# Optimization experiments

Measured on AMD Instinct MI355X. Metric: run time of the kernel, lower is better.

## Reference

```python
import jax, jax.numpy as jnp
import numpy as np

PRED, TOTAL, ITEM = 100000, 120000, 100000
NUI = PRED + ITEM            # nodes in user2item / reverse-consumption graphs
NODES = TOTAL + ITEM         # embedding table rows
EMB = 64
EPS = 1e-5


def _gatv2(src, dst, x, Wl, bl, Wr, br, attn, n):
    """DGL GATv2Conv (1 head), activation=leaky_relu(0.01)."""
    fs = x @ Wl + bl                                   # fc_src
    fd = x @ Wr + br                                   # fc_dst
    e = jax.nn.leaky_relu(fs[src] + fd[dst], 0.2) @ attn   # [E_edges]
    m = jax.ops.segment_max(e, dst, n)                 # per-dst max (stable softmax)
    ex = jnp.exp(e - m[dst])
    denom = jax.ops.segment_sum(ex, dst, n)
    alpha = ex / denom[dst]                            # edge softmax over in-edges
    out = jax.ops.segment_sum(alpha[:, None] * fs[src], dst, n)
    return jax.nn.leaky_relu(out, 0.01)


def _bn(x, g, b):
    mu = jnp.mean(x, 0)
    var = jnp.var(x, 0)
    return (x - mu) * jax.lax.rsqrt(var + EPS) * g + b


def _mlp(x, W, b, g, beta):
    # Linear -> BatchNorm1d (train mode, batch stats) -> LeakyReLU(0.01)
    return jax.nn.leaky_relu(_bn(x @ W + b, g, beta), 0.01)


def _cheb(src, dst, x, W, b, lam, n):
    """ChebConv order-3: h = sum_k T_k(Lhat) x @ W_k + b, leaky_relu."""
    deg = jnp.clip(jax.ops.segment_sum(jnp.ones_like(dst, jnp.float32), dst, n), 1.0)
    dinv = jax.lax.rsqrt(deg)
    norm = dinv[src] * dinv[dst]                       # D^-1/2 A D^-1/2 edge weight

    def lhat(v):  # (2/lam)(I - Ahat) v - v
        av = jax.ops.segment_sum(norm[:, None] * v[src], dst, n)
        return (2.0 / lam) * (v - av) - v

    T0 = x
    T1 = lhat(T0)
    T2 = 2.0 * lhat(T1) - T0
    return jax.nn.leaky_relu(T0 @ W[0] + T1 @ W[1] + T2 @ W[2] + b, 0.01)


def setup_inputs() -> dict:
    key = jax.random.key(0)
    ks = jax.random.split(key, 24)
    ri = lambda k, n, hi: jax.random.randint(k, (n,), 0, hi, dtype=jnp.int32)
    rn = lambda k, shp, s=0.1: jax.random.normal(k, shp, jnp.float32) * s
    return {
        "emb": rn(ks[0], (NODES, EMB), 1.0),
        "bn0_g": jnp.ones((EMB,), jnp.float32),
        "bn0_b": jnp.zeros((EMB,), jnp.float32),
        "gat_Wl": rn(ks[1], (5, EMB, EMB)),
        "gat_bl": jnp.zeros((5, EMB), jnp.float32),
        "gat_Wr": rn(ks[2], (5, EMB, EMB)),
        "gat_br": jnp.zeros((5, EMB), jnp.float32),
        "gat_attn": rn(ks[3], (5, EMB)),
        "cheb_W": rn(ks[4], (3, EMB, EMB)),
        "cheb_b": jnp.zeros((EMB,), jnp.float32),
        "mlp_W": rn(ks[5], (5, 2 * EMB, EMB)),
        "mlp_b": jnp.zeros((5, EMB), jnp.float32),
        "mlp_g": jnp.ones((5, EMB), jnp.float32),
        "mlp_beta": jnp.zeros((5, EMB), jnp.float32),
        "lambda_max": jnp.array([2.0], jnp.float32),
        "u2i_src": ri(ks[6], 1500000, NUI),
        "u2i_dst": ri(ks[7], 1500000, NUI),
        "rc_src": ri(ks[8], 1500000, NUI),
        "rc_dst": ri(ks[9], 1500000, NUI),
        "i2u_src": ri(ks[10], 1000000, PRED),
        "i2u_dst": ri(ks[11], 1000000, PRED),
        "i2u_ids": jnp.arange(PRED, dtype=jnp.int32),
        "sn_src": ri(ks[12], 1000000, PRED),
        "sn_dst": ri(ks[13], 1000000, PRED),
        "snn_src": ri(ks[14], 1500000, TOTAL),
        "snn_dst": ri(ks[15], 1500000, TOTAL),
    }


def reference(emb, bn0_g, bn0_b, gat_Wl, gat_bl, gat_Wr, gat_br, gat_attn,
              cheb_W, cheb_b, mlp_W, mlp_b, mlp_g, mlp_beta, lambda_max,
              u2i_src, u2i_dst, rc_src, rc_dst, i2u_src, i2u_dst, i2u_ids,
              sn_src, sn_dst, snn_src, snn_dst):
    gat = lambda i, src, dst, x, n: _gatv2(src, dst, x, gat_Wl[i], gat_bl[i],
                                           gat_Wr[i], gat_br[i], gat_attn[i], n)
    mlp = lambda i, x: _mlp(x, mlp_W[i], mlp_b[i], mlp_g[i], mlp_beta[i])

    e = _bn(emb, bn0_g, bn0_b)                        # embedding_BN over all nodes
    pred_u = e[:PRED]
    total_u = e[:TOTAL]
    item_e = e[-ITEM:]
    uie = jnp.concatenate([pred_u, item_e], axis=0)   # [NUI, EMB]

    # --- spatial attention: item influence branch ---
    u2i_emb = gat(0, u2i_src, u2i_dst, uie, NUI)
    iie = gat(1, rc_src, rc_dst, u2i_emb, NUI)[:PRED]

    # --- spatial attention: social item branch ---
    su = uie[i2u_ids]                                 # embedding[_ID]
    i2u_emb = gat(2, i2u_src, i2u_dst, su, PRED)
    soc = uie[:PRED]                                  # embedding[social_g.nodes()]
    mask = (jnp.sum(i2u_emb, axis=1) != 0)[:, None]
    soc = soc.at[i2u_ids].set(jnp.where(mask, i2u_emb, soc[i2u_ids]))
    sie = gat(3, sn_src, sn_dst, soc, PRED)

    user_item_embed = mlp(0, jnp.concatenate([iie, sie], axis=1))

    # --- spectral attention ---
    lam = lambda_max[0]
    h = _cheb(snn_src, snn_dst, total_u, cheb_W, cheb_b, lam, TOTAL)
    h = _cheb(snn_src, snn_dst, h, cheb_W, cheb_b, lam, TOTAL)
    user_social_embed = gat(4, snn_src, snn_dst, h, TOTAL)[:PRED]

    # --- mutualistic layer ---
    h_uP = mlp(1, jnp.concatenate([user_item_embed, pred_u], axis=1))
    h_uS = mlp(2, jnp.concatenate([user_social_embed, pred_u], axis=1))
    h_m = h_uP * h_uS
    h_mP = jnp.concatenate([h_m * jax.nn.softmax(h_uP, axis=1), h_uP], axis=1)
    h_mS = jnp.concatenate([h_m * jax.nn.softmax(h_uS, axis=1), h_uS], axis=1)

    # --- prediction layer ---
    h_new_P = mlp(3, h_mP)
    h_new_S = mlp(4, h_mS)
    return (h_new_P, h_new_S)
```

## Files before the change

### kernel.cpp

```cpp
#include <hip/hip_runtime.h>
#include <math.h>

static const int PRED  = 100000;
static const int TOTAL = 120000;
static const int ITEM  = 100000;
static const int NUI   = PRED + ITEM;
static const int NODES = TOTAL + ITEM;
#define BN_EPS 1e-5f
#define MNEG -1e30f
#define WNEG -2e30f

__device__ inline float lrelu(float v, float s) { return v > 0.f ? v : s * v; }

__global__ void k_bn_stats(const float* __restrict__ x, int n, float* __restrict__ sums) {
  __shared__ float ls[256], ls2[256];
  int t = threadIdx.x;
  int col = t & 63;
  float s = 0.f, s2 = 0.f;
  for (int r = blockIdx.x * 4 + (t >> 6); r < n; r += gridDim.x * 4) {
    float v = x[(size_t)r * 64 + col];
    s += v; s2 += v * v;
  }
  ls[t] = s; ls2[t] = s2;
  __syncthreads();
  if (t < 64) {
    atomicAdd(&sums[t],      ls[t] + ls[t + 64] + ls[t + 128] + ls[t + 192]);
    atomicAdd(&sums[64 + t], ls2[t] + ls2[t + 64] + ls2[t + 128] + ls2[t + 192]);
  }
}

__global__ void k_bn_apply(const float* __restrict__ x, float* __restrict__ y,
                           const float* __restrict__ sums,
                           const float* __restrict__ g, const float* __restrict__ b,
                           int n, int relu) {
  size_t tot = (size_t)n * 64;
  size_t i = (size_t)blockIdx.x * blockDim.x + threadIdx.x;
  size_t st = (size_t)gridDim.x * blockDim.x;
  float inv_n = 1.f / (float)n;
  for (; i < tot; i += st) {
    int c = (int)(i & 63);
    float mean = sums[c] * inv_n;
    float var = fmaxf(sums[64 + c] * inv_n - mean * mean, 0.f);
    float o = (x[i] - mean) * rsqrtf(var + BN_EPS) * g[c] + b[c];
    if (relu) o = lrelu(o, 0.01f);
    y[i] = o;
  }
}

__global__ void k_bn0_apply(const float* __restrict__ x, float* __restrict__ e_tot,
                            float* __restrict__ uie, const float* __restrict__ sums,
                            const float* __restrict__ g, const float* __restrict__ b) {
  size_t tot = (size_t)NODES * 64;
  size_t i = (size_t)blockIdx.x * blockDim.x + threadIdx.x;
  size_t st = (size_t)gridDim.x * blockDim.x;
  float inv_n = 1.f / (float)NODES;
  for (; i < tot; i += st) {
    int c = (int)(i & 63);
    size_t row = i >> 6;
    float mean = sums[c] * inv_n;
    float var = fmaxf(sums[64 + c] * inv_n - mean * mean, 0.f);
    float o = (x[i] - mean) * rsqrtf(var + BN_EPS) * g[c] + b[c];
    if (row < (size_t)TOTAL) e_tot[i] = o;
    else uie[((row - TOTAL) + PRED) * 64 + c] = o;
    if (row < (size_t)PRED) uie[i] = o;
  }
}

__global__ __launch_bounds__(128) void k_gemm_dual(const float* __restrict__ A,
    const float* __restrict__ Wl, const float* __restrict__ bl,
    const float* __restrict__ Wr, const float* __restrict__ br,
    float* __restrict__ FS, float* __restrict__ FD, int n) {
  __shared__ float As[128][65];
  __shared__ float Ws[64][68];
  int t = threadIdx.x;
  int row0 = blockIdx.x * 128;
  for (int i = t; i < 2048; i += 128) {
    int r = i >> 4, c = (i & 15) * 4, gr = row0 + r;
    float4 a;
    if (gr < n) a = *(const float4*)&A[(size_t)gr * 64 + c];
    else { a.x = a.y = a.z = a.w = 0.f; }
    As[r][c] = a.x; As[r][c + 1] = a.y; As[r][c + 2] = a.z; As[r][c + 3] = a.w;
  }
  int cg = (t & 7) * 8;
  int rg = (t >> 3) * 8;
  for (int s = 0; s < 2; ++s) {
    const float* Wm = s ? Wr : Wl;
    const float* bias = s ? br : bl;
    __syncthreads();
    for (int i = t; i < 4096; i += 128) Ws[i >> 6][i & 63] = Wm[i];
    __syncthreads();
    float bb[8];
    *(float4*)&bb[0] = *(const float4*)&bias[cg];
    *(float4*)&bb[4] = *(const float4*)&bias[cg + 4];
    float acc[8][8];
    #pragma unroll
    for (int i = 0; i < 8; ++i)
      #pragma unroll
      for (int j = 0; j < 8; ++j) acc[i][j] = bb[j];
    for (int k = 0; k < 64; ++k) {
      float w[8], a[8];
      *(float4*)&w[0] = *(const float4*)&Ws[k][cg];
      *(float4*)&w[4] = *(const float4*)&Ws[k][cg + 4];
      #pragma unroll
      for (int i = 0; i < 8; ++i) a[i] = As[rg + i][k];
      #pragma unroll
      for (int i = 0; i < 8; ++i)
        #pragma unroll
        for (int j = 0; j < 8; ++j)
          acc[i][j] += a[i] * w[j];
    }
    float* C = s ? FD : FS;
    #pragma unroll
    for (int i = 0; i < 8; ++i) {
      int gr = row0 + rg + i;
      if (gr < n) {
        float4 o0, o1;
        o0.x = acc[i][0]; o0.y = acc[i][1]; o0.z = acc[i][2]; o0.w = acc[i][3];
        o1.x = acc[i][4]; o1.y = acc[i][5]; o1.z = acc[i][6]; o1.w = acc[i][7];
        *(float4*)&C[(size_t)gr * 64 + cg] = o0;
        *(float4*)&C[(size_t)gr * 64 + cg + 4] = o1;
      }
    }
  }
}

__global__ __launch_bounds__(128) void k_gemm_cat(const float* __restrict__ A1,
    const float* __restrict__ A2, const float* __restrict__ A3,
    const float* __restrict__ Wm, const float* __restrict__ bias,
    float* __restrict__ C, int n, int nseg, int relu) {
  __shared__ float As[128][65];
  __shared__ float Ws[64][68];
  int t = threadIdx.x;
  int row0 = blockIdx.x * 128;
  int cg = (t & 7) * 8;
  int rg = (t >> 3) * 8;
  float bb[8];
  *(float4*)&bb[0] = *(const float4*)&bias[cg];
  *(float4*)&bb[4] = *(const float4*)&bias[cg + 4];
  float acc[8][8];
  #pragma unroll
  for (int i = 0; i < 8; ++i)
    #pragma unroll
    for (int j = 0; j < 8; ++j) acc[i][j] = bb[j];
  for (int s = 0; s < nseg; ++s) {
    const float* A = (s == 0) ? A1 : (s == 1) ? A2 : A3;
    __syncthreads();
    for (int i = t; i < 4096; i += 128) Ws[i >> 6][i & 63] = Wm[s * 4096 + i];
    for (int i = t; i < 2048; i += 128) {
      int r = i >> 4, c = (i & 15) * 4, gr = row0 + r;
      float4 a;
      if (gr < n) a = *(const float4*)&A[(size_t)gr * 64 + c];
      else { a.x = a.y = a.z = a.w = 0.f; }
      As[r][c] = a.x; As[r][c + 1] = a.y; As[r][c + 2] = a.z; As[r][c + 3] = a.w;
    }
    __syncthreads();
    for (int k = 0; k < 64; ++k) {
      float w[8], a[8];
      *(float4*)&w[0] = *(const float4*)&Ws[k][cg];
      *(float4*)&w[4] = *(const float4*)&Ws[k][cg + 4];
      #pragma unroll
      for (int i = 0; i < 8; ++i) a[i] = As[rg + i][k];
      #pragma unroll
      for (int i = 0; i < 8; ++i)
        #pragma unroll
        for (int j = 0; j < 8; ++j)
          acc[i][j] += a[i] * w[j];
    }
  }
  #pragma unroll
  for (int i = 0; i < 8; ++i) {
    int gr = row0 + rg + i;
    if (gr < n) {
      float4 o0, o1;
      o0.x = acc[i][0]; o0.y = acc[i][1]; o0.z = acc[i][2]; o0.w = acc[i][3];
      o1.x = acc[i][4]; o1.y = acc[i][5]; o1.z = acc[i][6]; o1.w = acc[i][7];
      if (relu) {
        o0.x = lrelu(o0.x, 0.01f); o0.y = lrelu(o0.y, 0.01f); o0.z = lrelu(o0.z, 0.01f); o0.w = lrelu(o0.w, 0.01f);
        o1.x = lrelu(o1.x, 0.01f); o1.y = lrelu(o1.y, 0.01f); o1.z = lrelu(o1.z, 0.01f); o1.w = lrelu(o1.w, 0.01f);
      }
      *(float4*)&C[(size_t)gr * 64 + cg] = o0;
      *(float4*)&C[(size_t)gr * 64 + cg + 4] = o1;
    }
  }
}

__global__ __launch_bounds__(512) void k_bhist(const int* __restrict__ dst, int* __restrict__ M,
                                               int E, int nbuck, int chunk) {
  __shared__ int h[1600];
  int t = threadIdx.x, b = blockIdx.x;
  for (int k = t; k < nbuck; k += 512) h[k] = 0;
  __syncthreads();
  int beg = b * chunk, end = min(E, beg + chunk);
  for (int i = beg + t; i < end; i += 512) atomicAdd(&h[dst[i] >> 7], 1);
  __syncthreads();
  for (int k = t; k < nbuck; k += 512) M[k * 64 + b] = h[k];
}

__global__ void k_scan_part(const int* __restrict__ counts, int* __restrict__ bsums, int n) {
  __shared__ int sh[256];
  int t = threadIdx.x;
  int i = blockIdx.x * 256 + t;
  sh[t] = (i < n) ? counts[i] : 0;
  __syncthreads();
  for (int o = 128; o; o >>= 1) {
    if (t < o) sh[t] += sh[t + o];
    __syncthreads();
  }
  if (t == 0) bsums[blockIdx.x] = sh[0];
}

__global__ void k_scan_tops(int* __restrict__ bsums, int nb) {
  __shared__ int sh[256];
  int t = threadIdx.x;
  int carry = 0;
  for (int base = 0; base < nb; base += 256) {
    int i = base + t;
    int v = (i < nb) ? bsums[i] : 0;
    __syncthreads();
    sh[t] = v;
    __syncthreads();
    for (int o = 1; o < 256; o <<= 1) {
      int tv = (t >= o) ? sh[t - o] : 0;
      __syncthreads();
      sh[t] += tv;
      __syncthreads();
    }
    int incl = sh[t];
    int total = sh[255];
    if (i < nb) bsums[i] = incl - v + carry;
    carry += total;
  }
}

__global__ void k_scan_apply_ip(int* __restrict__ cnts, const int* __restrict__ bsums, int n) {
  __shared__ int sh[256];
  int t = threadIdx.x;
  int i = blockIdx.x * 256 + t;
  int v = (i < n) ? cnts[i] : 0;
  sh[t] = v;
  __syncthreads();
  for (int o = 1; o < 256; o <<= 1) {
    int tv = (t >= o) ? sh[t - o] : 0;
    __syncthreads();
    sh[t] += tv;
    __syncthreads();
  }
  if (i < n) cnts[i] = sh[t] - v + bsums[blockIdx.x];
}

__global__ __launch_bounds__(512) void k_bscatter(const int* __restrict__ src, const int* __restrict__ dst,
                                                  const int* __restrict__ M, unsigned int* __restrict__ tmp,
                                                  int E, int nbuck, int chunk) {
  __shared__ int cur[1600];
  int t = threadIdx.x, b = blockIdx.x;
  for (int k = t; k < nbuck; k += 512) cur[k] = M[k * 64 + b];
  __syncthreads();
  int beg = b * chunk, end = min(E, beg + chunk);
  for (int i = beg + t; i < end; i += 512) {
    int d = dst[i];
    int pos = atomicAdd(&cur[d >> 7], 1);
    tmp[pos] = ((unsigned int)(d & 127) << 25) | (unsigned int)src[i];
  }
}

__global__ __launch_bounds__(256) void k_bfinal(const unsigned int* __restrict__ tmp,
                                                const int* __restrict__ M,
                                                int* __restrict__ offs, int* __restrict__ csr,
                                                int E, int nbuck, int n) {
  __shared__ int h[128];
  int t = threadIdx.x, k = blockIdx.x;
  int base = M[k * 64];
  int next = (k + 1 < nbuck) ? M[(k + 1) * 64] : E;
  if (t < 128) h[t] = 0;
  __syncthreads();
  for (int i = base + t; i < next; i += 256) atomicAdd(&h[tmp[i] >> 25], 1);
  __syncthreads();
  if (t == 0) { int s = 0; for (int j = 0; j < 128; ++j) { int c = h[j]; h[j] = s; s += c; } }
  __syncthreads();
  int r0 = k << 7;
  if (t < 128 && r0 + t < n) offs[r0 + t] = base + h[t];
  if (k == nbuck - 1 && t == 0) offs[n] = E;
  __syncthreads();
  for (int i = base + t; i < next; i += 256) {
    unsigned int v = tmp[i];
    int rl = (int)(v >> 25);
    int pos = base + atomicAdd(&h[rl], 1);
    csr[pos] = (int)(v & 0x01FFFFFFu);
  }
}

__global__ void k_dinv(const int* __restrict__ offs, float* __restrict__ dinv, int n) {
  int i = blockIdx.x * blockDim.x + threadIdx.x;
  int st = gridDim.x * blockDim.x;
  for (; i < n; i += st) dinv[i] = rsqrtf(fmaxf((float)(offs[i + 1] - offs[i]), 1.f));
}

__global__ __launch_bounds__(256) void k_gat_fused(const float* __restrict__ fs,
                                                   const float* __restrict__ fd,
                                                   const float* __restrict__ attn,
                                                   const int* __restrict__ offs,
                                                   const int* __restrict__ csr_src,
                                                   float* __restrict__ out, int n) {
  int lane = threadIdx.x & 63;
  int g  = lane >> 4;
  int li = lane & 15;
  int c4 = li * 4;
  int wid = (blockIdx.x * blockDim.x + threadIdx.x) >> 6;
  int nw = (gridDim.x * blockDim.x) >> 6;
  float4 ak = *(const float4*)&attn[c4];
  for (int r = wid; r < n; r += nw) {
    int beg = offs[r], end = offs[r + 1];
    float4 fdv = *(const float4*)&fd[(size_t)r * 64 + c4];
    float m = MNEG, den = 0.f;
    float4 acc; acc.x = acc.y = acc.z = acc.w = 0.f;
    for (int e4 = beg; e4 < end; e4 += 4) {
      int myE = e4 + g;
      bool act = myE < end;
      int s = act ? csr_src[myE] : 0;
      float4 fsv = *(const float4*)&fs[(size_t)s * 64 + c4];
      float w = ak.x * lrelu(fsv.x + fdv.x, 0.2f)
              + ak.y * lrelu(fsv.y + fdv.y, 0.2f)
              + ak.z * lrelu(fsv.z + fdv.z, 0.2f)
              + ak.w * lrelu(fsv.w + fdv.w, 0.2f);
      w += __shfl_xor(w, 1);
      w += __shfl_xor(w, 2);
      w += __shfl_xor(w, 4);
      w += __shfl_xor(w, 8);
      if (!act) w = WNEG;
      float nm = fmaxf(m, w);
      float sc = __expf(m - nm);
      float p  = __expf(w - nm);
      den = den * sc + p;
      acc.x = acc.x * sc + p * fsv.x;
      acc.y = acc.y * sc + p * fsv.y;
      acc.z = acc.z * sc + p * fsv.z;
      acc.w = acc.w * sc + p * fsv.w;
      m = nm;
    }
    #pragma unroll
    for (int o = 16; o < 64; o <<= 1) {
      float mo   = __shfl_xor(m, o);
      float deno = __shfl_xor(den, o);
      float ax = __shfl_xor(acc.x, o);
      float ay = __shfl_xor(acc.y, o);
      float az = __shfl_xor(acc.z, o);
      float aw = __shfl_xor(acc.w, o);
      float nm = fmaxf(m, mo);
      float sc = __expf(m - nm);
      float so = __expf(mo - nm);
      den = den * sc + deno * so;
      acc.x = acc.x * sc + ax * so;
      acc.y = acc.y * sc + ay * so;
      acc.z = acc.z * sc + az * so;
      acc.w = acc.w * sc + aw * so;
      m = nm;
    }
    if (g == 0) {
      float inv = (end > beg) ? 1.f / den : 0.f;
      float4 o4;
      o4.x = lrelu(acc.x * inv, 0.01f);
      o4.y = lrelu(acc.y * inv, 0.01f);
      o4.z = lrelu(acc.z * inv, 0.01f);
      o4.w = lrelu(acc.w * inv, 0.01f);
      *(float4*)&out[(size_t)r * 64 + c4] = o4;
    }
  }
}

__global__ __launch_bounds__(256) void k_cheb_fused(const float* __restrict__ v,
                                                    const float* __restrict__ t0,
                                                    const float* __restrict__ dinv,
                                                    const int* __restrict__ offs,
                                                    const int* __restrict__ csr_src,
                                                    float* __restrict__ out,
                                                    const float* __restrict__ lamf,
                                                    int n, int mode) {
  int lane = threadIdx.x & 63;
  int g  = lane >> 4;
  int li = lane & 15;
  int c4 = li * 4;
  int wid = (blockIdx.x * blockDim.x + threadIdx.x) >> 6;
  int nw = (gridDim.x * blockDim.x) >> 6;
  float cc = 2.f / lamf[0];
  for (int r = wid; r < n; r += nw) {
    int beg = offs[r], end = offs[r + 1];
    float dr = dinv[r];
    float4 acc; acc.x = acc.y = acc.z = acc.w = 0.f;
    for (int e4 = beg; e4 < end; e4 += 4) {
      int myE = e4 + g;
      bool act = myE < end;
      int s = act ? csr_src[myE] : 0;
      float ns = act ? dinv[s] * dr : 0.f;
      float4 vv = *(const float4*)&v[(size_t)s * 64 + c4];
      acc.x += ns * vv.x;
      acc.y += ns * vv.y;
      acc.z += ns * vv.z;
      acc.w += ns * vv.w;
    }
    #pragma unroll
    for (int o = 16; o < 64; o <<= 1) {
      acc.x += __shfl_xor(acc.x, o);
      acc.y += __shfl_xor(acc.y, o);
      acc.z += __shfl_xor(acc.z, o);
      acc.w += __shfl_xor(acc.w, o);
    }
    if (g == 0) {
      float4 vr = *(const float4*)&v[(size_t)r * 64 + c4];
      float4 o4;
      o4.x = cc * (vr.x - acc.x) - vr.x;
      o4.y = cc * (vr.y - acc.y) - vr.y;
      o4.z = cc * (vr.z - acc.z) - vr.z;
      o4.w = cc * (vr.w - acc.w) - vr.w;
      if (mode == 2) {
        float4 t = *(const float4*)&t0[(size_t)r * 64 + c4];
        o4.x = 2.f * o4.x - t.x;
        o4.y = 2.f * o4.y - t.y;
        o4.z = 2.f * o4.z - t.z;
        o4.w = 2.f * o4.w - t.w;
      }
      *(float4*)&out[(size_t)r * 64 + c4] = o4;
    }
  }
}

__global__ void k_mask_select(const float* __restrict__ i2u, const float* __restrict__ pred,
                              float* __restrict__ out, int n) {
  int lane = threadIdx.x & 63;
  int wid = (blockIdx.x * blockDim.x + threadIdx.x) >> 6;
  int nw = (gridDim.x * blockDim.x) >> 6;
  for (int r = wid; r < n; r += nw) {
    float v = i2u[(size_t)r * 64 + lane];
    float s = v;
    for (int o = 32; o; o >>= 1) s += __shfl_xor(s, o);
    out[(size_t)r * 64 + lane] = (s != 0.f) ? v : pred[(size_t)r * 64 + lane];
  }
}

__global__ void k_softmax_mul(const float* __restrict__ a, const float* __restrict__ b,
                              float* __restrict__ out, int n) {
  int lane = threadIdx.x & 63;
  int wid = (blockIdx.x * blockDim.x + threadIdx.x) >> 6;
  int nw = (gridDim.x * blockDim.x) >> 6;
  for (int r = wid; r < n; r += nw) {
    size_t idx = (size_t)r * 64 + lane;
    float av = a[idx];
    float mx = av;
    for (int o = 32; o; o >>= 1) mx = fmaxf(mx, __shfl_xor(mx, o));
    float e = expf(av - mx);
    float s = e;
    for (int o = 32; o; o >>= 1) s += __shfl_xor(s, o);
    out[idx] = av * b[idx] * (e / s);
  }
}

extern "C" void kernel_launch(void* const* d_in, const int* in_sizes, int n_in,
                              void* d_out, int out_size, void* d_ws, size_t ws_size,
                              hipStream_t stream) {
  const float* emb      = (const float*)d_in[0];
  const float* bn0_g    = (const float*)d_in[1];
  const float* bn0_b    = (const float*)d_in[2];
  const float* gat_Wl   = (const float*)d_in[3];
  const float* gat_bl   = (const float*)d_in[4];
  const float* gat_Wr   = (const float*)d_in[5];
  const float* gat_br   = (const float*)d_in[6];
  const float* gat_attn = (const float*)d_in[7];
  const float* cheb_W   = (const float*)d_in[8];
  const float* cheb_b   = (const float*)d_in[9];
  const float* mlp_W    = (const float*)d_in[10];
  const float* mlp_b    = (const float*)d_in[11];
  const float* mlp_g    = (const float*)d_in[12];
  const float* mlp_beta = (const float*)d_in[13];
  const float* lam      = (const float*)d_in[14];
  const int* u2i_src = (const int*)d_in[15];
  const int* u2i_dst = (const int*)d_in[16];
  const int* rc_src  = (const int*)d_in[17];
  const int* rc_dst  = (const int*)d_in[18];
  const int* i2u_src = (const int*)d_in[19];
  const int* i2u_dst = (const int*)d_in[20];
  const int* sn_src  = (const int*)d_in[22];
  const int* sn_dst  = (const int*)d_in[23];
  const int* snn_src = (const int*)d_in[24];
  const int* snn_dst = (const int*)d_in[25];
  int E_u2i = in_sizes[15], E_rc = in_sizes[17], E_i2u = in_sizes[19];
  int E_sn = in_sizes[22], E_snn = in_sizes[24];

  float* Wp = (float*)d_ws;
  size_t off = 0;
  auto alloc = [&](size_t nf) { float* p = Wp + off; off += nf; return p; };
  float* e_tot = alloc((size_t)TOTAL * 64);
  float* POOL  = alloc((size_t)600000 * 64);
  int*   csr_src = (int*)alloc(1500000);
  int*   offs    = (int*)alloc(200064);
  float* spare   = alloc(200064);
  int*   bsums   = (int*)alloc(1024);
  float* dinv  = alloc(TOTAL);
  float* sums  = alloc(128);

  auto R = [&](size_t row) { return POOL + row * 64; };
  unsigned int* tmp_e = (unsigned int*)R(520000);
  int*          Mbuf  = (int*)R(545000);
  (void)spare;

  float* outP = (float*)d_out;
  float* outS = outP + (size_t)PRED * 64;

  auto stats = [&](const float* x, int n) {
    hipMemsetAsync(sums, 0, 128 * 4, stream);
    k_bn_stats<<<512, 256, 0, stream>>>(x, n, sums);
  };
  auto build_csr = [&](const int* src, const int* dst, int E, int n) {
    int nbuck = (n + 127) >> 7;
    int chunk = (E + 63) / 64;
    int L = nbuck * 64;
    int NB = (L + 255) / 256;
    k_bhist<<<64, 512, 0, stream>>>(dst, Mbuf, E, nbuck, chunk);
    k_scan_part<<<NB, 256, 0, stream>>>(Mbuf, bsums, L);
    k_scan_tops<<<1, 256, 0, stream>>>(bsums, NB);
    k_scan_apply_ip<<<NB, 256, 0, stream>>>(Mbuf, bsums, L);
    k_bscatter<<<64, 512, 0, stream>>>(src, dst, Mbuf, tmp_e, E, nbuck, chunk);
    k_bfinal<<<nbuck, 256, 0, stream>>>(tmp_e, Mbuf, offs, csr_src, E, nbuck, n);
  };
  auto gat = [&](int i, const float* fs, const float* fd, int n, float* out) {
    k_gat_fused<<<(n + 3) / 4, 256, 0, stream>>>(fs, fd, gat_attn + i * 64, offs, csr_src, out, n);
  };
  auto gat_gemms = [&](int i, const float* A, float* fs, float* fd, int n) {
    k_gemm_dual<<<(n + 127) / 128, 128, 0, stream>>>(A, gat_Wl + i * 4096, gat_bl + i * 64,
                                                     gat_Wr + i * 4096, gat_br + i * 64, fs, fd, n);
  };
  auto cat2 = [&](const float* A1, const float* A2, const float* Wm, const float* bias,
                  float* C, int n) {
    k_gemm_cat<<<(n + 127) / 128, 128, 0, stream>>>(A1, A2, nullptr, Wm, bias, C, n, 2, 0);
  };

  stats(emb, NODES);
  k_bn0_apply<<<2048, 256, 0, stream>>>(emb, e_tot, R(0), sums, bn0_g, bn0_b);

  build_csr(u2i_src, u2i_dst, E_u2i, NUI);
  gat_gemms(0, R(0), R(200000), R(400000), NUI);
  gat(0, R(200000), R(400000), NUI, R(0));

  build_csr(rc_src, rc_dst, E_rc, NUI);
  gat_gemms(1, R(0), R(200000), R(400000), NUI);
  gat(1, R(200000), R(400000), NUI, R(0));

  build_csr(i2u_src, i2u_dst, E_i2u, PRED);
  gat_gemms(2, e_tot, R(200000), R(400000), PRED);
  gat(2, R(200000), R(400000), PRED, R(300000));

  k_mask_select<<<2048, 256, 0, stream>>>(R(300000), e_tot, R(400000), PRED);

  build_csr(sn_src, sn_dst, E_sn, PRED);
  gat_gemms(3, R(400000), R(200000), R(500000), PRED);
  gat(3, R(200000), R(500000), PRED, R(300000));

  cat2(R(0), R(300000), mlp_W + 0 * 8192, mlp_b + 0, R(100000), PRED);
  stats(R(100000), PRED);
  k_bn_apply<<<2048, 256, 0, stream>>>(R(100000), R(0), sums, mlp_g + 0, mlp_beta + 0, PRED, 1);

  build_csr(snn_src, snn_dst, E_snn, TOTAL);
  k_dinv<<<256, 256, 0, stream>>>(offs, dinv, TOTAL);

  auto cheb = [&](const float* T0, float* T1, float* T2, float* outC) {
    k_cheb_fused<<<(TOTAL + 3) / 4, 256, 0, stream>>>(T0, T0, dinv, offs, csr_src, T1, lam, TOTAL, 1);
    k_cheb_fused<<<(TOTAL + 3) / 4, 256, 0, stream>>>(T1, T0, dinv, offs, csr_src, T2, lam, TOTAL, 2);
    k_gemm_cat<<<(TOTAL + 127) / 128, 128, 0, stream>>>(T0, T1, T2, cheb_W, cheb_b, outC, TOTAL, 3, 1);
  };
  cheb(e_tot, R(100000), R(220000), R(340000));
  cheb(R(340000), R(100000), R(220000), R(460000));

  gat_gemms(4, R(460000), R(100000), R(220000), TOTAL);
  gat(4, R(100000), R(220000), TOTAL, R(460000));

  cat2(R(0), e_tot, mlp_W + 1 * 8192, mlp_b + 64, R(100000), PRED);
  stats(R(100000), PRED);
  k_bn_apply<<<2048, 256, 0, stream>>>(R(100000), R(100000), sums, mlp_g + 64, mlp_beta + 64, PRED, 1);

  cat2(R(460000), e_tot, mlp_W + 2 * 8192, mlp_b + 128, R(200000), PRED);
  stats(R(200000), PRED);
  k_bn_apply<<<2048, 256, 0, stream>>>(R(200000), R(200000), sums, mlp_g + 128, mlp_beta + 128, PRED, 1);

  k_softmax_mul<<<2048, 256, 0, stream>>>(R(100000), R(200000), R(300000), PRED);
  cat2(R(300000), R(100000), mlp_W + 3 * 8192, mlp_b + 192, R(400000), PRED);
  stats(R(400000), PRED);
  k_bn_apply<<<2048, 256, 0, stream>>>(R(400000), outP, sums, mlp_g + 192, mlp_beta + 192, PRED, 1);

  k_softmax_mul<<<2048, 256, 0, stream>>>(R(200000), R(100000), R(300000), PRED);
  cat2(R(300000), R(200000), mlp_W + 4 * 8192, mlp_b + 256, R(400000), PRED);
  stats(R(400000), PRED);
  k_bn_apply<<<2048, 256, 0, stream>>>(R(400000), outS, sums, mlp_g + 256, mlp_beta + 256, PRED, 1);
}
```

Measured before the change: 2.331 ms.

## Fuse BatchNorm stats into concat GEMM epilogue and drop GAT softmax max-tracking

The concat GEMM epilogue now accumulates per-column sum and sum-of-squares in shared memory and atomically adds them to the global stats buffer. This removes the separate stats kernel that re-read each 100k x 64 MLP output. Separately, the GAT edge softmax no longer tracks a running max: it exponentiates raw scores and sums them directly, which simplifies the inner loop and the cross-group reduction. The unshifted exponent can overflow for large attention scores, so correctness depends on score magnitudes staying small.

```diff
diff --git a/kernel.cpp b/kernel.cpp
--- a/kernel.cpp
+++ b/kernel.cpp
@@ -7,8 +7,6 @@
 static const int NUI   = PRED + ITEM;
 static const int NODES = TOTAL + ITEM;
 #define BN_EPS 1e-5f
-#define MNEG -1e30f
-#define WNEG -2e30f
 
 __device__ inline float lrelu(float v, float s) { return v > 0.f ? v : s * v; }
 
@@ -127,9 +125,10 @@
 __global__ __launch_bounds__(128) void k_gemm_cat(const float* __restrict__ A1,
     const float* __restrict__ A2, const float* __restrict__ A3,
     const float* __restrict__ Wm, const float* __restrict__ bias,
-    float* __restrict__ C, int n, int nseg, int relu) {
+    float* __restrict__ C, int n, int nseg, int relu, float* __restrict__ stats) {
   __shared__ float As[128][65];
   __shared__ float Ws[64][68];
+  __shared__ float st[128];
   int t = threadIdx.x;
   int row0 = blockIdx.x * 128;
   int cg = (t & 7) * 8;
@@ -167,20 +166,39 @@
           acc[i][j] += a[i] * w[j];
     }
   }
+  float csum[8], csq[8];
+  #pragma unroll
+  for (int j = 0; j < 8; ++j) { csum[j] = 0.f; csq[j] = 0.f; }
   #pragma unroll
   for (int i = 0; i < 8; ++i) {
     int gr = row0 + rg + i;
     if (gr < n) {
+      #pragma unroll
+      for (int j = 0; j < 8; ++j) {
+        float o = acc[i][j];
+        if (relu) o = lrelu(o, 0.01f);
+        acc[i][j] = o;
+        csum[j] += o;
+        csq[j] += o * o;
+      }
       float4 o0, o1;
       o0.x = acc[i][0]; o0.y = acc[i][1]; o0.z = acc[i][2]; o0.w = acc[i][3];
       o1.x = acc[i][4]; o1.y = acc[i][5]; o1.z = acc[i][6]; o1.w = acc[i][7];
-      if (relu) {
-        o0.x = lrelu(o0.x, 0.01f); o0.y = lrelu(o0.y, 0.01f); o0.z = lrelu(o0.z, 0.01f); o0.w = lrelu(o0.w, 0.01f);
-        o1.x = lrelu(o1.x, 0.01f); o1.y = lrelu(o1.y, 0.01f); o1.z = lrelu(o1.z, 0.01f); o1.w = lrelu(o1.w, 0.01f);
-      }
       *(float4*)&C[(size_t)gr * 64 + cg] = o0;
       *(float4*)&C[(size_t)gr * 64 + cg + 4] = o1;
     }
+  }
+  if (stats) {
+    __syncthreads();
+    st[t] = 0.f;
+    __syncthreads();
+    #pragma unroll
+    for (int j = 0; j < 8; ++j) {
+      atomicAdd(&st[cg + j], csum[j]);
+      atomicAdd(&st[64 + cg + j], csq[j]);
+    }
+    __syncthreads();
+    atomicAdd(&stats[t], st[t]);
   }
 }
 
@@ -311,7 +329,7 @@
   for (int r = wid; r < n; r += nw) {
     int beg = offs[r], end = offs[r + 1];
     float4 fdv = *(const float4*)&fd[(size_t)r * 64 + c4];
-    float m = MNEG, den = 0.f;
+    float den = 0.f;
     float4 acc; acc.x = acc.y = acc.z = acc.w = 0.f;
     for (int e4 = beg; e4 < end; e4 += 4) {
       int myE = e4 + g;
@@ -326,34 +344,20 @@
       w += __shfl_xor(w, 2);
       w += __shfl_xor(w, 4);
       w += __shfl_xor(w, 8);
-      if (!act) w = WNEG;
-      float nm = fmaxf(m, w);
-      float sc = __expf(m - nm);
-      float p  = __expf(w - nm);
-      den = den * sc + p;
-      acc.x = acc.x * sc + p * fsv.x;
-      acc.y = acc.y * sc + p * fsv.y;
-      acc.z = acc.z * sc + p * fsv.z;
-      acc.w = acc.w * sc + p * fsv.w;
-      m = nm;
+      float p = act ? __expf(w) : 0.f;
+      den += p;
+      acc.x += p * fsv.x;
+      acc.y += p * fsv.y;
+      acc.z += p * fsv.z;
+      acc.w += p * fsv.w;
     }
     #pragma unroll
     for (int o = 16; o < 64; o <<= 1) {
-      float mo   = __shfl_xor(m, o);
-      float deno = __shfl_xor(den, o);
-      float ax = __shfl_xor(acc.x, o);
-      float ay = __shfl_xor(acc.y, o);
-      float az = __shfl_xor(acc.z, o);
-      float aw = __shfl_xor(acc.w, o);
-      float nm = fmaxf(m, mo);
-      float sc = __expf(m - nm);
-      float so = __expf(mo - nm);
-      den = den * sc + deno * so;
-      acc.x = acc.x * sc + ax * so;
-      acc.y = acc.y * sc + ay * so;
-      acc.z = acc.z * sc + az * so;
-      acc.w = acc.w * sc + aw * so;
-      m = nm;
+      den   += __shfl_xor(den, o);
+      acc.x += __shfl_xor(acc.x, o);
+      acc.y += __shfl_xor(acc.y, o);
+      acc.z += __shfl_xor(acc.z, o);
+      acc.w += __shfl_xor(acc.w, o);
     }
     if (g == 0) {
       float inv = (end > beg) ? 1.f / den : 0.f;
@@ -504,10 +508,6 @@
   float* outP = (float*)d_out;
   float* outS = outP + (size_t)PRED * 64;
 
-  auto stats = [&](const float* x, int n) {
-    hipMemsetAsync(sums, 0, 128 * 4, stream);
-    k_bn_stats<<<512, 256, 0, stream>>>(x, n, sums);
-  };
   auto build_csr = [&](const int* src, const int* dst, int E, int n) {
     int nbuck = (n + 127) >> 7;
     int chunk = (E + 63) / 64;
@@ -527,12 +527,14 @@
     k_gemm_dual<<<(n + 127) / 128, 128, 0, stream>>>(A, gat_Wl + i * 4096, gat_bl + i * 64,
                                                      gat_Wr + i * 4096, gat_br + i * 64, fs, fd, n);
   };
-  auto cat2 = [&](const float* A1, const float* A2, const float* Wm, const float* bias,
-                  float* C, int n) {
-    k_gemm_cat<<<(n + 127) / 128, 128, 0, stream>>>(A1, A2, nullptr, Wm, bias, C, n, 2, 0);
+  auto cat2s = [&](const float* A1, const float* A2, const float* Wm, const float* bias,
+                   float* C, int n) {
+    hipMemsetAsync(sums, 0, 128 * 4, stream);
+    k_gemm_cat<<<(n + 127) / 128, 128, 0, stream>>>(A1, A2, nullptr, Wm, bias, C, n, 2, 0, sums);
   };
 
-  stats(emb, NODES);
+  hipMemsetAsync(sums, 0, 128 * 4, stream);
+  k_bn_stats<<<512, 256, 0, stream>>>(emb, NODES, sums);
   k_bn0_apply<<<2048, 256, 0, stream>>>(emb, e_tot, R(0), sums, bn0_g, bn0_b);
 
   build_csr(u2i_src, u2i_dst, E_u2i, NUI);
@@ -553,8 +555,7 @@
   gat_gemms(3, R(400000), R(200000), R(500000), PRED);
   gat(3, R(200000), R(500000), PRED, R(300000));
 
-  cat2(R(0), R(300000), mlp_W + 0 * 8192, mlp_b + 0, R(100000), PRED);
-  stats(R(100000), PRED);
+  cat2s(R(0), R(300000), mlp_W + 0 * 8192, mlp_b + 0, R(100000), PRED);
   k_bn_apply<<<2048, 256, 0, stream>>>(R(100000), R(0), sums, mlp_g + 0, mlp_beta + 0, PRED, 1);
 
   build_csr(snn_src, snn_dst, E_snn, TOTAL);
@@ -563,7 +564,7 @@
   auto cheb = [&](const float* T0, float* T1, float* T2, float* outC) {
     k_cheb_fused<<<(TOTAL + 3) / 4, 256, 0, stream>>>(T0, T0, dinv, offs, csr_src, T1, lam, TOTAL, 1);
     k_cheb_fused<<<(TOTAL + 3) / 4, 256, 0, stream>>>(T1, T0, dinv, offs, csr_src, T2, lam, TOTAL, 2);
-    k_gemm_cat<<<(TOTAL + 127) / 128, 128, 0, stream>>>(T0, T1, T2, cheb_W, cheb_b, outC, TOTAL, 3, 1);
+    k_gemm_cat<<<(TOTAL + 127) / 128, 128, 0, stream>>>(T0, T1, T2, cheb_W, cheb_b, outC, TOTAL, 3, 1, nullptr);
   };
   cheb(e_tot, R(100000), R(220000), R(340000));
   cheb(R(340000), R(100000), R(220000), R(460000));
@@ -571,21 +572,17 @@
   gat_gemms(4, R(460000), R(100000), R(220000), TOTAL);
   gat(4, R(100000), R(220000), TOTAL, R(460000));
 
-  cat2(R(0), e_tot, mlp_W + 1 * 8192, mlp_b + 64, R(100000), PRED);
-  stats(R(100000), PRED);
+  cat2s(R(0), e_tot, mlp_W + 1 * 8192, mlp_b + 64, R(100000), PRED);
   k_bn_apply<<<2048, 256, 0, stream>>>(R(100000), R(100000), sums, mlp_g + 64, mlp_beta + 64, PRED, 1);
 
-  cat2(R(460000), e_tot, mlp_W + 2 * 8192, mlp_b + 128, R(200000), PRED);
-  stats(R(200000), PRED);
+  cat2s(R(460000), e_tot, mlp_W + 2 * 8192, mlp_b + 128, R(200000), PRED);
   k_bn_apply<<<2048, 256, 0, stream>>>(R(200000), R(200000), sums, mlp_g + 128, mlp_beta + 128, PRED, 1);
 
   k_softmax_mul<<<2048, 256, 0, stream>>>(R(100000), R(200000), R(300000), PRED);
-  cat2(R(300000), R(100000), mlp_W + 3 * 8192, mlp_b + 192, R(400000), PRED);
-  stats(R(400000), PRED);
+  cat2s(R(300000), R(100000), mlp_W + 3 * 8192, mlp_b + 192, R(400000), PRED);
   k_bn_apply<<<2048, 256, 0, stream>>>(R(400000), outP, sums, mlp_g + 192, mlp_beta + 192, PRED, 1);
 
   k_softmax_mul<<<2048, 256, 0, stream>>>(R(200000), R(100000), R(300000), PRED);
-  cat2(R(300000), R(200000), mlp_W + 4 * 8192, mlp_b + 256, R(400000), PRED);
-  stats(R(400000), PRED);
+  cat2s(R(300000), R(200000), mlp_W + 4 * 8192, mlp_b + 256, R(400000), PRED);
   k_bn_apply<<<2048, 256, 0, stream>>>(R(400000), outS, sums, mlp_g + 256, mlp_beta + 256, PRED, 1);
 }
```

Result: no change. 2.357 ms (+1.1%).
